# Kernel tuning notes

Measured on AMD Instinct MI355X. Metric: run time of the kernel, lower is better.

## Reference

```python
import jax, jax.numpy as jnp
import numpy as np

BETA = 0.25

def setup_inputs() -> dict:
    key = jax.random.key(0)
    k1, k2 = jax.random.split(key)
    z = jax.random.normal(k1, (4096, 64, 64), dtype=jnp.float32)
    codebooks = jax.random.normal(k2, (64, 256, 64), dtype=jnp.float32)
    return {"z": z, "codebooks": codebooks}

def reference(z, codebooks):
    # z: (B, M, d); codebooks: (M, K, d)
    B, M, d = z.shape
    # squared distances (B, M, K) via ||z||^2 - 2 z.c + ||c||^2 (avoids (B,M,K,d) blowup)
    z2 = jnp.sum(z * z, axis=-1)                      # (B, M)
    c2 = jnp.sum(codebooks * codebooks, axis=-1)      # (M, K)
    zc = jnp.einsum('bmd,mkd->bmk', z, codebooks)     # (B, M, K)
    distances = z2[:, :, None] - 2.0 * zc + c2[None]  # (B, M, K)
    encoding_indices = jnp.argmin(distances, axis=-1) # (B, M) int
    # per-subspace codebook gather: codebooks[m, idx[b, m], :]
    quantized_raw = codebooks[jnp.arange(M)[None, :], encoding_indices]  # (B, M, d)
    # straight-through estimator
    quantized = z + jax.lax.stop_gradient(quantized_raw - z)
    q_loss = (BETA * jnp.mean((jax.lax.stop_gradient(quantized) - z) ** 2)
              + jnp.mean((quantized - jax.lax.stop_gradient(z)) ** 2))
    return quantized, encoding_indices, q_loss
```

## Files before the change

kernel.cpp:

```cpp
#include <hip/hip_runtime.h>

#define IDX_BASE 16777216UL
#define LOSS_IDX 17039360UL
#define EPS2 0.02f

typedef float4 f4;
typedef _Float16 half8 __attribute__((ext_vector_type(8)));
typedef float f32x4 __attribute__((ext_vector_type(4)));

static __device__ __forceinline__ unsigned umax(unsigned a, unsigned b) { return a > b ? a : b; }
static __device__ __forceinline__ unsigned umin(unsigned a, unsigned b) { return a < b ? a : b; }
static __device__ __forceinline__ unsigned f2mono(float s) {
    unsigned u = __float_as_uint(s);
    return u ^ (unsigned)(((int)u >> 31) | 0x80000000);
}
static __device__ __forceinline__ float mono2f(unsigned v) {
    return __uint_as_float(v ^ (((unsigned)((int)(~v) >> 31)) | 0x80000000u));
}

__global__ __launch_bounds__(256) void pq_frag(const float* __restrict__ cb,
                                               half8* __restrict__ fragbuf,
                                               float* __restrict__ c2) {
    int bx = blockIdx.x, tid = threadIdx.x;
    int m = bx >> 2, sub = bx & 3;
    int w = tid >> 6, lane = tid & 63, lh = lane >> 4, l15 = lane & 15;
    const float* cbm = cb + (size_t)m * (256 * 64);
    half8* fbm = fragbuf + (size_t)m * (16 * 4 * 64);
    int tile = w * 4 + sub;
    int code = tile * 16 + l15;
    const float* crow = cbm + code * 64 + lh * 8;
    float ss = 0.f;
    #pragma unroll
    for (int s = 0; s < 2; ++s) {
        f4 a = *reinterpret_cast<const f4*>(crow + s * 32);
        f4 b = *reinterpret_cast<const f4*>(crow + s * 32 + 4);
        float v[8] = {a.x, a.y, a.z, a.w, b.x, b.y, b.z, b.w};
        half8 hi, lo;
        #pragma unroll
        for (int e = 0; e < 8; ++e) {
            _Float16 h = (_Float16)v[e];
            hi[e] = h; lo[e] = (_Float16)(v[e] - (float)h);
            ss = fmaf(v[e], v[e], ss);
        }
        fbm[(tile * 4 + s * 2 + 0) * 64 + lane] = hi;
        fbm[(tile * 4 + s * 2 + 1) * 64 + lane] = lo;
    }
    ss += __shfl_xor(ss, 16, 64);
    ss += __shfl_xor(ss, 32, 64);
    if (lh == 0) c2[m * 256 + code] = ss;
}

__global__ __launch_bounds__(256, 3) void pq_main(
    const float* __restrict__ z, const float* __restrict__ cb,
    const float* __restrict__ c2ws, const half8* __restrict__ fragbuf,
    float* __restrict__ out, float* __restrict__ partial)
{
    __shared__ int   sBest[256];
    __shared__ float sW[4];

    const int tid = threadIdx.x, bx = blockIdx.x;
    const int m = ((bx & 7) << 3) | ((bx >> 3) & 7);
    const int chunk = bx >> 6;
    const int w = tid >> 6, lane = tid & 63;
    const int lh = lane >> 4, l15 = lane & 15;
    const int rowbase = chunk * 256 + w * 64;
    const unsigned payBase = 255u - (unsigned)(lh * 4);

    const float* __restrict__ cbm = cb + (size_t)m * (256 * 64);
    const f4* cb4m = reinterpret_cast<const f4*>(cbm);
    const half8* __restrict__ fb = fragbuf + (size_t)m * (16 * 4 * 64);
    const f4* __restrict__ c2t = reinterpret_cast<const f4*>(c2ws + m * 256);

    half8 zh[4][2], zl[4][2];
    #pragma unroll
    for (int h = 0; h < 4; ++h) {
        size_t rh = (size_t)(rowbase + h * 16 + l15);
        const float* zb = z + (rh * 64 + m) * 64 + lh * 8;
        f4 p0 = *reinterpret_cast<const f4*>(zb);
        f4 p1 = *reinterpret_cast<const f4*>(zb + 4);
        f4 p2 = *reinterpret_cast<const f4*>(zb + 32);
        f4 p3 = *reinterpret_cast<const f4*>(zb + 36);
        float v0[8] = {p0.x,p0.y,p0.z,p0.w,p1.x,p1.y,p1.z,p1.w};
        float v1[8] = {p2.x,p2.y,p2.z,p2.w,p3.x,p3.y,p3.z,p3.w};
        #pragma unroll
        for (int e = 0; e < 8; ++e) {
            _Float16 a = (_Float16)v0[e];
            zh[h][0][e] = a; zl[h][0][e] = (_Float16)(v0[e] - (float)a);
            _Float16 b = (_Float16)v1[e];
            zh[h][1][e] = b; zl[h][1][e] = (_Float16)(v1[e] - (float)b);
        }
    }

    unsigned K1[4] = {0, 0, 0, 0}, K2[4] = {0, 0, 0, 0};

    #pragma unroll 2
    for (int tile = 0; tile < 16; ++tile) {
        half8 ah0 = fb[(tile * 4 + 0) * 64 + lane];
        half8 al0 = fb[(tile * 4 + 1) * 64 + lane];
        half8 ah1 = fb[(tile * 4 + 2) * 64 + lane];
        half8 al1 = fb[(tile * 4 + 3) * 64 + lane];
        f4 cv = c2t[tile * 4 + lh];
        f32x4 ci; ci[0] = -0.5f*cv.x; ci[1] = -0.5f*cv.y; ci[2] = -0.5f*cv.z; ci[3] = -0.5f*cv.w;
        #pragma unroll
        for (int h = 0; h < 4; ++h) {
            f32x4 acc = ci;
            acc = __builtin_amdgcn_mfma_f32_16x16x32_f16(ah0, zh[h][0], acc, 0, 0, 0);
            acc = __builtin_amdgcn_mfma_f32_16x16x32_f16(ah1, zh[h][1], acc, 0, 0, 0);
            acc = __builtin_amdgcn_mfma_f32_16x16x32_f16(ah0, zl[h][0], acc, 0, 0, 0);
            acc = __builtin_amdgcn_mfma_f32_16x16x32_f16(ah1, zl[h][1], acc, 0, 0, 0);
            acc = __builtin_amdgcn_mfma_f32_16x16x32_f16(al0, zh[h][0], acc, 0, 0, 0);
            acc = __builtin_amdgcn_mfma_f32_16x16x32_f16(al1, zh[h][1], acc, 0, 0, 0);
            unsigned kk0 = (f2mono(acc[0]) & 0xFFFFFF00u) | (payBase - (unsigned)(tile * 16 + 0));
            unsigned kk1 = (f2mono(acc[1]) & 0xFFFFFF00u) | (payBase - (unsigned)(tile * 16 + 1));
            unsigned kk2 = (f2mono(acc[2]) & 0xFFFFFF00u) | (payBase - (unsigned)(tile * 16 + 2));
            unsigned kk3 = (f2mono(acc[3]) & 0xFFFFFF00u) | (payBase - (unsigned)(tile * 16 + 3));
            unsigned a  = umax(kk0, kk1), b2 = umin(kk0, kk1);
            unsigned c  = umax(kk2, kk3), d  = umin(kk2, kk3);
            unsigned t1 = umax(a, c);
            unsigned t2 = umax(umin(a, c), umax(b2, d));
            K2[h] = umax(umax(K2[h], t2), umin(K1[h], t1));
            K1[h] = umax(K1[h], t1);
        }
    }

    #pragma unroll
    for (int h = 0; h < 4; ++h) {
        #pragma unroll
        for (int off = 16; off <= 32; off <<= 1) {
            unsigned o1 = (unsigned)__shfl_xor((int)K1[h], off, 64);
            unsigned o2 = (unsigned)__shfl_xor((int)K2[h], off, 64);
            K2[h] = umax(umax(K2[h], o2), umin(K1[h], o1));
            K1[h] = umax(K1[h], o1);
        }
        int cd = 255 - (int)(K1[h] & 0xFFu);
        float s1 = mono2f(K1[h] & 0xFFFFFF00u);
        float s2 = mono2f(K2[h] & 0xFFFFFF00u);
        bool need = (s1 - s2) < EPS2;
        unsigned mask = (unsigned)(__ballot(need)) & 0xFFFFu;
        while (mask) {
            int row = __builtin_ctz(mask); mask &= mask - 1;
            size_t rg = (size_t)(rowbase + h * 16 + row);
            const f4* zr4 = reinterpret_cast<const f4*>(z + (rg * 64 + m) * 64);
            float bs = -1e30f; int bkx = 0;
            #pragma unroll 1
            for (int j = 0; j < 4; ++j) {
                int k = j * 64 + lane;
                float s = -0.5f * c2ws[m * 256 + k];
                #pragma unroll
                for (int d4 = 0; d4 < 16; ++d4) {
                    f4 cc = cb4m[k * 16 + d4];
                    f4 zz = zr4[d4];
                    s = fmaf(zz.x, cc.x, s); s = fmaf(zz.y, cc.y, s);
                    s = fmaf(zz.z, cc.z, s); s = fmaf(zz.w, cc.w, s);
                }
                if (s > bs) { bs = s; bkx = k; }
            }
            #pragma unroll
            for (int off = 1; off < 64; off <<= 1) {
                float ov = __shfl_xor(bs, off, 64);
                int   ok = __shfl_xor(bkx, off, 64);
                if (ov > bs || (ov == bs && ok < bkx)) { bs = ov; bkx = ok; }
            }
            if (l15 == row) cd = bkx;
        }
        if (lane < 16) sBest[w * 64 + h * 16 + lane] = cd;
    }
    __syncthreads();

    float lsum = 0.f;
    #pragma unroll
    for (int it = 0; it < 2; ++it) {
        int row = it * 128 + (tid >> 1);
        int hf  = tid & 1;
        int k   = sBest[row];
        size_t b = (size_t)(chunk * 256 + row);
        const f4* q4 = cb4m + (size_t)k * 16 + hf * 8;
        const f4* z4 = reinterpret_cast<const f4*>(z + (b * 64 + m) * 64) + hf * 8;
        f4*       o4 = reinterpret_cast<f4*>(out + (b * 64 + m) * 64) + hf * 8;
        float l0 = 0.f, l1 = 0.f;
        #pragma unroll
        for (int c = 0; c < 8; ++c) {
            f4 qv = q4[c], zv = z4[c];
            o4[c] = qv;
            float d0 = qv.x - zv.x, d1 = qv.y - zv.y, d2 = qv.z - zv.z, d3 = qv.w - zv.w;
            l0 = fmaf(d0, d0, l0); l1 = fmaf(d1, d1, l1);
            l0 = fmaf(d2, d2, l0); l1 = fmaf(d3, d3, l1);
        }
        lsum += l0 + l1;
    }
    out[IDX_BASE + (size_t)(chunk * 256 + tid) * 64 + m] = (float)sBest[tid];

    #pragma unroll
    for (int off = 1; off < 64; off <<= 1) lsum += __shfl_xor(lsum, off, 64);
    if (lane == 0) sW[w] = lsum;
    __syncthreads();
    if (tid == 0) partial[bx] = (sW[0] + sW[1]) + (sW[2] + sW[3]);
}

__global__ __launch_bounds__(256) void pq_loss(const float* __restrict__ partial,
                                               float* __restrict__ out)
{
    __shared__ float sW[4];
    float s = (partial[threadIdx.x]       + partial[threadIdx.x + 256])
            + (partial[threadIdx.x + 512] + partial[threadIdx.x + 768]);
    #pragma unroll
    for (int off = 1; off < 64; off <<= 1) s += __shfl_xor(s, off, 64);
    if ((threadIdx.x & 63) == 0) sW[threadIdx.x >> 6] = s;
    __syncthreads();
    if (threadIdx.x == 0)
        out[LOSS_IDX] = ((sW[0] + sW[1]) + (sW[2] + sW[3])) * (1.25f / 16777216.0f);
}

extern "C" void kernel_launch(void* const* d_in, const int* in_sizes, int n_in,
                              void* d_out, int out_size, void* d_ws, size_t ws_size,
                              hipStream_t stream) {
    const float* zp  = (const float*)d_in[0];
    const float* cbp = (const float*)d_in[1];
    float* outp = (float*)d_out;
    float* c2ws = (float*)d_ws;
    half8* frag = (half8*)((float*)d_ws + 16384);
    float* part = (float*)d_ws + 16384 + 1048576;

    pq_frag<<<dim3(256),  dim3(256), 0, stream>>>(cbp, frag, c2ws);
    pq_main<<<dim3(1024), dim3(256), 0, stream>>>(zp, cbp, c2ws, frag, outp, part);
    pq_loss<<<dim3(1),    dim3(256), 0, stream>>>(part, outp);
}
```

Baseline: 97.32 us.

## Use single-wave blocks and fuse gather/loss into each wave, dropping LDS sync

Splits the main kernel into 4096 single-wavefront blocks of 64 rows each, removing shared memory and __syncthreads. Each wave gathers its own codebook rows, writes the quantized output and indices directly from the MFMA layout, and computes the loss using the z values reconstructed from the fp16 hi/lo splits already held in registers, so z is not reloaded. The tile loop unroll rises to 4 and the loss reduction reads 4096 partials. The risks are less coalesced output writes, a slightly different loss value because z is rebuilt from fp16 halves, and more blocks to schedule.

```diff
diff --git a/kernel.cpp b/kernel.cpp
--- a/kernel.cpp
+++ b/kernel.cpp
@@ -50,21 +50,16 @@
     if (lh == 0) c2[m * 256 + code] = ss;
 }
 
-__global__ __launch_bounds__(256, 3) void pq_main(
+__global__ __launch_bounds__(64, 4) void pq_main(
     const float* __restrict__ z, const float* __restrict__ cb,
     const float* __restrict__ c2ws, const half8* __restrict__ fragbuf,
     float* __restrict__ out, float* __restrict__ partial)
 {
-    __shared__ int   sBest[256];
-    __shared__ float sW[4];
-
-    const int tid = threadIdx.x, bx = blockIdx.x;
+    const int bx = blockIdx.x, lane = threadIdx.x;
     const int m = ((bx & 7) << 3) | ((bx >> 3) & 7);
     const int chunk = bx >> 6;
-    const int w = tid >> 6, lane = tid & 63;
+    const int rowbase = chunk * 64;
     const int lh = lane >> 4, l15 = lane & 15;
-    const int rowbase = chunk * 256 + w * 64;
-    const unsigned payBase = 255u - (unsigned)(lh * 4);
 
     const float* __restrict__ cbm = cb + (size_t)m * (256 * 64);
     const f4* cb4m = reinterpret_cast<const f4*>(cbm);
@@ -73,8 +68,8 @@
 
     half8 zh[4][2], zl[4][2];
     #pragma unroll
-    for (int h = 0; h < 4; ++h) {
-        size_t rh = (size_t)(rowbase + h * 16 + l15);
+    for (int rt = 0; rt < 4; ++rt) {
+        size_t rh = (size_t)(rowbase + rt * 16 + l15);
         const float* zb = z + (rh * 64 + m) * 64 + lh * 8;
         f4 p0 = *reinterpret_cast<const f4*>(zb);
         f4 p1 = *reinterpret_cast<const f4*>(zb + 4);
@@ -85,15 +80,15 @@
         #pragma unroll
         for (int e = 0; e < 8; ++e) {
             _Float16 a = (_Float16)v0[e];
-            zh[h][0][e] = a; zl[h][0][e] = (_Float16)(v0[e] - (float)a);
+            zh[rt][0][e] = a; zl[rt][0][e] = (_Float16)(v0[e] - (float)a);
             _Float16 b = (_Float16)v1[e];
-            zh[h][1][e] = b; zl[h][1][e] = (_Float16)(v1[e] - (float)b);
-        }
-    }
-
-    unsigned K1[4] = {0, 0, 0, 0}, K2[4] = {0, 0, 0, 0};
-
-    #pragma unroll 2
+            zh[rt][1][e] = b; zl[rt][1][e] = (_Float16)(v1[e] - (float)b);
+        }
+    }
+
+    unsigned K1[4] = {0u,0u,0u,0u}, K2[4] = {0u,0u,0u,0u};
+
+    #pragma unroll 4
     for (int tile = 0; tile < 16; ++tile) {
         half8 ah0 = fb[(tile * 4 + 0) * 64 + lane];
         half8 al0 = fb[(tile * 4 + 1) * 64 + lane];
@@ -101,45 +96,47 @@
         half8 al1 = fb[(tile * 4 + 3) * 64 + lane];
         f4 cv = c2t[tile * 4 + lh];
         f32x4 ci; ci[0] = -0.5f*cv.x; ci[1] = -0.5f*cv.y; ci[2] = -0.5f*cv.z; ci[3] = -0.5f*cv.w;
-        #pragma unroll
-        for (int h = 0; h < 4; ++h) {
+        const unsigned pb = 255u - (unsigned)(tile * 16 + lh * 4);
+        #pragma unroll
+        for (int rt = 0; rt < 4; ++rt) {
             f32x4 acc = ci;
-            acc = __builtin_amdgcn_mfma_f32_16x16x32_f16(ah0, zh[h][0], acc, 0, 0, 0);
-            acc = __builtin_amdgcn_mfma_f32_16x16x32_f16(ah1, zh[h][1], acc, 0, 0, 0);
-            acc = __builtin_amdgcn_mfma_f32_16x16x32_f16(ah0, zl[h][0], acc, 0, 0, 0);
-            acc = __builtin_amdgcn_mfma_f32_16x16x32_f16(ah1, zl[h][1], acc, 0, 0, 0);
-            acc = __builtin_amdgcn_mfma_f32_16x16x32_f16(al0, zh[h][0], acc, 0, 0, 0);
-            acc = __builtin_amdgcn_mfma_f32_16x16x32_f16(al1, zh[h][1], acc, 0, 0, 0);
-            unsigned kk0 = (f2mono(acc[0]) & 0xFFFFFF00u) | (payBase - (unsigned)(tile * 16 + 0));
-            unsigned kk1 = (f2mono(acc[1]) & 0xFFFFFF00u) | (payBase - (unsigned)(tile * 16 + 1));
-            unsigned kk2 = (f2mono(acc[2]) & 0xFFFFFF00u) | (payBase - (unsigned)(tile * 16 + 2));
-            unsigned kk3 = (f2mono(acc[3]) & 0xFFFFFF00u) | (payBase - (unsigned)(tile * 16 + 3));
+            acc = __builtin_amdgcn_mfma_f32_16x16x32_f16(ah0, zh[rt][0], acc, 0, 0, 0);
+            acc = __builtin_amdgcn_mfma_f32_16x16x32_f16(ah1, zh[rt][1], acc, 0, 0, 0);
+            acc = __builtin_amdgcn_mfma_f32_16x16x32_f16(ah0, zl[rt][0], acc, 0, 0, 0);
+            acc = __builtin_amdgcn_mfma_f32_16x16x32_f16(ah1, zl[rt][1], acc, 0, 0, 0);
+            acc = __builtin_amdgcn_mfma_f32_16x16x32_f16(al0, zh[rt][0], acc, 0, 0, 0);
+            acc = __builtin_amdgcn_mfma_f32_16x16x32_f16(al1, zh[rt][1], acc, 0, 0, 0);
+            unsigned kk0 = (f2mono(acc[0]) & 0xFFFFFF00u) | (pb - 0u);
+            unsigned kk1 = (f2mono(acc[1]) & 0xFFFFFF00u) | (pb - 1u);
+            unsigned kk2 = (f2mono(acc[2]) & 0xFFFFFF00u) | (pb - 2u);
+            unsigned kk3 = (f2mono(acc[3]) & 0xFFFFFF00u) | (pb - 3u);
             unsigned a  = umax(kk0, kk1), b2 = umin(kk0, kk1);
             unsigned c  = umax(kk2, kk3), d  = umin(kk2, kk3);
             unsigned t1 = umax(a, c);
             unsigned t2 = umax(umin(a, c), umax(b2, d));
-            K2[h] = umax(umax(K2[h], t2), umin(K1[h], t1));
-            K1[h] = umax(K1[h], t1);
-        }
-    }
-
-    #pragma unroll
-    for (int h = 0; h < 4; ++h) {
+            K2[rt] = umax(umax(K2[rt], t2), umin(K1[rt], t1));
+            K1[rt] = umax(K1[rt], t1);
+        }
+    }
+
+    float lsum = 0.f;
+    #pragma unroll
+    for (int rt = 0; rt < 4; ++rt) {
         #pragma unroll
         for (int off = 16; off <= 32; off <<= 1) {
-            unsigned o1 = (unsigned)__shfl_xor((int)K1[h], off, 64);
-            unsigned o2 = (unsigned)__shfl_xor((int)K2[h], off, 64);
-            K2[h] = umax(umax(K2[h], o2), umin(K1[h], o1));
-            K1[h] = umax(K1[h], o1);
-        }
-        int cd = 255 - (int)(K1[h] & 0xFFu);
-        float s1 = mono2f(K1[h] & 0xFFFFFF00u);
-        float s2 = mono2f(K2[h] & 0xFFFFFF00u);
+            unsigned o1 = (unsigned)__shfl_xor((int)K1[rt], off, 64);
+            unsigned o2 = (unsigned)__shfl_xor((int)K2[rt], off, 64);
+            K2[rt] = umax(umax(K2[rt], o2), umin(K1[rt], o1));
+            K1[rt] = umax(K1[rt], o1);
+        }
+        int cd = 255 - (int)(K1[rt] & 0xFFu);
+        float s1 = mono2f(K1[rt] & 0xFFFFFF00u);
+        float s2 = mono2f(K2[rt] & 0xFFFFFF00u);
         bool need = (s1 - s2) < EPS2;
         unsigned mask = (unsigned)(__ballot(need)) & 0xFFFFu;
         while (mask) {
             int row = __builtin_ctz(mask); mask &= mask - 1;
-            size_t rg = (size_t)(rowbase + h * 16 + row);
+            size_t rg = (size_t)(rowbase + rt * 16 + row);
             const f4* zr4 = reinterpret_cast<const f4*>(z + (rg * 64 + m) * 64);
             float bs = -1e30f; int bkx = 0;
             #pragma unroll 1
@@ -163,46 +160,41 @@
             }
             if (l15 == row) cd = bkx;
         }
-        if (lane < 16) sBest[w * 64 + h * 16 + lane] = cd;
-    }
-    __syncthreads();
-
-    float lsum = 0.f;
-    #pragma unroll
-    for (int it = 0; it < 2; ++it) {
-        int row = it * 128 + (tid >> 1);
-        int hf  = tid & 1;
-        int k   = sBest[row];
-        size_t b = (size_t)(chunk * 256 + row);
-        const f4* q4 = cb4m + (size_t)k * 16 + hf * 8;
-        const f4* z4 = reinterpret_cast<const f4*>(z + (b * 64 + m) * 64) + hf * 8;
-        f4*       o4 = reinterpret_cast<f4*>(out + (b * 64 + m) * 64) + hf * 8;
-        float l0 = 0.f, l1 = 0.f;
-        #pragma unroll
-        for (int c = 0; c < 8; ++c) {
-            f4 qv = q4[c], zv = z4[c];
-            o4[c] = qv;
-            float d0 = qv.x - zv.x, d1 = qv.y - zv.y, d2 = qv.z - zv.z, d3 = qv.w - zv.w;
-            l0 = fmaf(d0, d0, l0); l1 = fmaf(d1, d1, l1);
-            l0 = fmaf(d2, d2, l0); l1 = fmaf(d3, d3, l1);
-        }
-        lsum += l0 + l1;
-    }
-    out[IDX_BASE + (size_t)(chunk * 256 + tid) * 64 + m] = (float)sBest[tid];
+        {
+            size_t rg = (size_t)(rowbase + rt * 16 + l15);
+            const f4* qb = cb4m + (size_t)cd * 16 + lh * 2;
+            f4 q0 = qb[0], q1 = qb[1], q2 = qb[8], q3 = qb[9];
+            float* ob = out + (rg * 64 + m) * 64 + lh * 8;
+            *reinterpret_cast<f4*>(ob)      = q0;
+            *reinterpret_cast<f4*>(ob + 4)  = q1;
+            *reinterpret_cast<f4*>(ob + 32) = q2;
+            *reinterpret_cast<f4*>(ob + 36) = q3;
+            float qq0[8] = {q0.x,q0.y,q0.z,q0.w,q1.x,q1.y,q1.z,q1.w};
+            float qq1[8] = {q2.x,q2.y,q2.z,q2.w,q3.x,q3.y,q3.z,q3.w};
+            #pragma unroll
+            for (int e = 0; e < 8; ++e) {
+                float zr0 = (float)zh[rt][0][e] + (float)zl[rt][0][e];
+                float zr1 = (float)zh[rt][1][e] + (float)zl[rt][1][e];
+                float d0 = qq0[e] - zr0, d1 = qq1[e] - zr1;
+                lsum = fmaf(d0, d0, lsum); lsum = fmaf(d1, d1, lsum);
+            }
+            if (lane < 16)
+                out[IDX_BASE + (size_t)(rowbase + rt * 16 + lane) * 64 + m] = (float)cd;
+        }
+    }
 
     #pragma unroll
     for (int off = 1; off < 64; off <<= 1) lsum += __shfl_xor(lsum, off, 64);
-    if (lane == 0) sW[w] = lsum;
-    __syncthreads();
-    if (tid == 0) partial[bx] = (sW[0] + sW[1]) + (sW[2] + sW[3]);
+    if (lane == 0) partial[bx] = lsum;
 }
 
 __global__ __launch_bounds__(256) void pq_loss(const float* __restrict__ partial,
                                                float* __restrict__ out)
 {
     __shared__ float sW[4];
-    float s = (partial[threadIdx.x]       + partial[threadIdx.x + 256])
-            + (partial[threadIdx.x + 512] + partial[threadIdx.x + 768]);
+    float s = 0.f;
+    #pragma unroll
+    for (int i = 0; i < 16; ++i) s += partial[threadIdx.x + i * 256];
     #pragma unroll
     for (int off = 1; off < 64; off <<= 1) s += __shfl_xor(s, off, 64);
     if ((threadIdx.x & 63) == 0) sW[threadIdx.x >> 6] = s;
@@ -222,6 +214,6 @@
     float* part = (float*)d_ws + 16384 + 1048576;
 
     pq_frag<<<dim3(256),  dim3(256), 0, stream>>>(cbp, frag, c2ws);
-    pq_main<<<dim3(1024), dim3(256), 0, stream>>>(zp, cbp, c2ws, frag, outp, part);
+    pq_main<<<dim3(4096), dim3(64),  0, stream>>>(zp, cbp, c2ws, frag, outp, part);
     pq_loss<<<dim3(1),    dim3(256), 0, stream>>>(part, outp);
 }
```

After: 103.6 us. 1.06x slower.
